# Performance work log

Measured on AMD Instinct MI355X. Metric: run time of the kernel, lower is better.

The kernel has to match this reference:

```python
import jax, jax.numpy as jnp
import numpy as np

B, N, C = 2, 2048, 768
H = 12
D = C // H
WINDOW = 129  # odd; half-window = 64
SCALE = D ** -0.5


def setup_inputs() -> dict:
    key = jax.random.key(0)
    k_x, k_qkv, k_proj, k_pb = jax.random.split(key, 4)
    x = jax.random.normal(k_x, (B, N, C), dtype=jnp.float32)
    # nn.Linear weights: stored as [out, in]; qkv_bias=False so no qkv bias
    w_qkv = jax.random.normal(k_qkv, (3 * C, C), dtype=jnp.float32) * (C ** -0.5)
    w_proj = jax.random.normal(k_proj, (C, C), dtype=jnp.float32) * (C ** -0.5)
    b_proj = jax.random.normal(k_pb, (C,), dtype=jnp.float32) * 0.01
    return {"x": x, "w_qkv": w_qkv, "w_proj": w_proj, "b_proj": b_proj}


def reference(x, w_qkv, w_proj, b_proj):
    b, n, c = x.shape
    # qkv projection: [B,N,3C] -> [3,B,H,N,D]
    qkv = jnp.einsum('bnc,ec->bne', x, w_qkv)
    qkv = qkv.reshape(b, n, 3, H, D).transpose(2, 0, 3, 1, 4)
    q, k, v = qkv[0], qkv[1], qkv[2]
    # dense scores then sliding-window mask (faithful to source)
    attn = jnp.einsum('bhnd,bhmd->bhnm', q, k) * SCALE
    half = WINDOW // 2
    idx = jnp.arange(n)
    mask = jnp.abs(idx[:, None] - idx[None, :]) <= half  # [N,N]
    attn = jnp.where(mask[None, None], attn, -jnp.inf)
    attn = jax.nn.softmax(attn, axis=-1)
    attn = jnp.nan_to_num(attn)
    out = jnp.einsum('bhnm,bhmd->bhnd', attn, v)  # [B,H,N,D]
    out = out.transpose(0, 2, 1, 3).reshape(b, n, c)
    out = jnp.einsum('bnc,oc->bno', out, w_proj) + b_proj
    return out
```

## Files before the change

kernel.cpp:

```cpp
#include <hip/hip_runtime.h>
#include <hip/hip_bf16.h>

#define Bsz   2
#define Nseq  2048
#define Cdim  768
#define E3    2304
#define Hh    12
#define Dd    64
#define HALF  64
#define SCALEF 0.125f

typedef __attribute__((ext_vector_type(8))) short short8;
typedef __attribute__((ext_vector_type(4))) float f32x4;

__device__ __forceinline__ unsigned short f2bf(float f) {
    unsigned int u = __float_as_uint(f);
    u = (u + 0x7FFFu + ((u >> 16) & 1u)) >> 16;
    return (unsigned short)u;
}
__device__ __forceinline__ unsigned int pk2(float a, float b) {
    __hip_bfloat162 h = __float22bfloat162_rn(make_float2(a, b));
    union { __hip_bfloat162 h2; unsigned int u; } cv; cv.h2 = h; return cv.u;
}
__device__ __forceinline__ uint4 cvt8(const float4& lo, const float4& hi) {
    return make_uint4(pk2(lo.x, lo.y), pk2(lo.z, lo.w),
                      pk2(hi.x, hi.y), pk2(hi.z, hi.w));
}

__device__ __forceinline__ void gl_lds16(const unsigned short* g, unsigned short* l) {
    __builtin_amdgcn_global_load_lds(
        (__attribute__((address_space(1))) void*)(g),
        (__attribute__((address_space(3))) void*)(l), 16, 0, 0);
}

__global__ __launch_bounds__(256) void cvt3(
    const float* __restrict__ x, const float* __restrict__ wq,
    const float* __restrict__ wp, unsigned short* __restrict__ xb,
    unsigned short* __restrict__ wqb, unsigned short* __restrict__ wpb)
{
    const int gid = blockIdx.x * 256 + threadIdx.x;
    const float* src; unsigned short* dst; int off;
    if (gid < 393216)      { src = x;  dst = xb;  off = gid; }
    else if (gid < 614400) { src = wq; dst = wqb; off = gid - 393216; }
    else                   { src = wp; dst = wpb; off = gid - 614400; }
    const float4 lo = *(const float4*)&src[(size_t)off * 8];
    const float4 hi = *(const float4*)&src[(size_t)off * 8 + 4];
    *(uint4*)&dst[(size_t)off * 8] = cvt8(lo, hi);
}

__global__ __launch_bounds__(256) void qkv_mfma(
    const unsigned short* __restrict__ xb, const unsigned short* __restrict__ wqb,
    unsigned short* __restrict__ qkvb)
{
    __shared__ __align__(16) unsigned short smem[16384];
    unsigned short* Asm = smem;
    unsigned short* Bsm = smem + 8192;

    const int t  = threadIdx.x;
    const int id = blockIdx.y * 18 + blockIdx.x;
    const int p8 = id & 7, j8 = id >> 3;
    const int wg = p8 * 72 + j8;
    const int by = wg / 18, bx = wg % 18;
    const int row0 = by * 128, col0 = bx * 128;

    const int lane = t & 63, wave = t >> 6;
    const int wm = wave >> 1, wn = wave & 1;
    const int ln = lane & 15, quad = lane >> 4;
    const int lr  = lane >> 3;
    const int sc  = ((lane ^ lr) & 7) * 8;
    const int xsw = (ln & 7) << 3;

    f32x4 acc[4][4] = {};

    for (int k0 = 0; k0 < Cdim; k0 += 64) {
        __syncthreads();
#pragma unroll
        for (int j = 0; j < 4; ++j) {
            gl_lds16(&xb[(size_t)(row0 + wave*32 + j*8 + lr) * Cdim + k0 + sc],
                     &Asm[(wave*4 + j) * 512]);
            gl_lds16(&wqb[(size_t)(col0 + wave*32 + j*8 + lr) * Cdim + k0 + sc],
                     &Bsm[(wave*4 + j) * 512]);
        }
        __syncthreads();
#pragma unroll
        for (int kk = 0; kk < 2; ++kk) {
            short8 af[4], bf[4];
#pragma unroll
            for (int mi = 0; mi < 4; ++mi)
                af[mi] = *(const short8*)&Asm[(wm*64 + mi*16 + ln)*64
                                              + ((kk*32 + quad*8) ^ xsw)];
#pragma unroll
            for (int ni = 0; ni < 4; ++ni)
                bf[ni] = *(const short8*)&Bsm[(wn*64 + ni*16 + ln)*64
                                              + ((kk*32 + quad*8) ^ xsw)];
#pragma unroll
            for (int mi = 0; mi < 4; ++mi)
#pragma unroll
                for (int ni = 0; ni < 4; ++ni)
                    acc[mi][ni] = __builtin_amdgcn_mfma_f32_16x16x32_bf16(
                        af[mi], bf[ni], acc[mi][ni], 0, 0, 0);
        }
    }

    unsigned short (*Cs)[72] = (unsigned short(*)[72])smem;
    const int rA = t >> 3, c8 = t & 7;
#pragma unroll
    for (int p = 0; p < 2; ++p) {
        __syncthreads();
        if (wn == p) {
#pragma unroll
            for (int mi = 0; mi < 4; ++mi)
#pragma unroll
                for (int ni = 0; ni < 4; ++ni)
#pragma unroll
                    for (int reg = 0; reg < 4; ++reg)
                        Cs[wm*64 + mi*16 + quad*4 + reg][ni*16 + ln] =
                            f2bf(acc[mi][ni][reg]);
        }
        __syncthreads();
#pragma unroll
        for (int j = 0; j < 4; ++j)
            *(uint4*)&qkvb[(size_t)(row0 + rA + j*32) * E3 + col0 + p*64 + c8*8] =
                *(const uint4*)&Cs[rA + j*32][c8*8];
    }
}

__global__ __launch_bounds__(256) void proj_mfma(
    const unsigned short* __restrict__ Ab, const unsigned short* __restrict__ wpb,
    const float* __restrict__ bias, float* __restrict__ out)
{
    __shared__ __align__(16) unsigned short smem[8192];
    unsigned short* Asm = smem;
    unsigned short* Bsm = smem + 4096;

    const int t  = threadIdx.x;
    const int id = blockIdx.y * 12 + blockIdx.x;
    const int p8 = id & 7, j2 = id >> 3;
    const int bx = j2 % 12;
    const int by = p8 * 8 + j2 / 12;
    const int row0 = by * 64, col0 = bx * 64;

    const int lane = t & 63, wave = t >> 6;
    const int ln = lane & 15, quad = lane >> 4;
    const int lr  = lane >> 3;
    const int sc  = ((lane ^ lr) & 7) * 8;
    const int xsw = (ln & 7) << 3;

    f32x4 acc[4] = {};

    for (int k0 = 0; k0 < Cdim; k0 += 64) {
        __syncthreads();
#pragma unroll
        for (int j = 0; j < 2; ++j) {
            const int r = wave*16 + j*8 + lr;
            gl_lds16(&Ab[(size_t)(row0 + r) * Cdim + k0 + sc],
                     &Asm[(wave*2 + j) * 512]);
            gl_lds16(&wpb[(size_t)(col0 + r) * Cdim + k0 + sc],
                     &Bsm[(wave*2 + j) * 512]);
        }
        __syncthreads();
#pragma unroll
        for (int kc = 0; kc < 2; ++kc) {
            short8 af = *(const short8*)&Asm[(wave*16 + ln)*64
                                             + ((kc*32 + quad*8) ^ xsw)];
#pragma unroll
            for (int ni = 0; ni < 4; ++ni) {
                short8 bf = *(const short8*)&Bsm[(ni*16 + ln)*64
                                                 + ((kc*32 + quad*8) ^ xsw)];
                acc[ni] = __builtin_amdgcn_mfma_f32_16x16x32_bf16(af, bf, acc[ni], 0, 0, 0);
            }
        }
    }

    float (*Csf)[36] = (float(*)[36])smem;
#pragma unroll
    for (int p = 0; p < 2; ++p) {
        __syncthreads();
#pragma unroll
        for (int ni = 0; ni < 2; ++ni) {
            const int nn = p * 2 + ni;
#pragma unroll
            for (int reg = 0; reg < 4; ++reg)
                Csf[wave*16 + quad*4 + reg][ni*16 + ln] = acc[nn][reg];
        }
        __syncthreads();
#pragma unroll
        for (int j = 0; j < 2; ++j) {
            const int F = t + j * 256, r = F >> 3, c4 = F & 7;
            const int col = col0 + p * 32 + c4 * 4;
            float4 v  = *(const float4*)&Csf[r][c4 * 4];
            float4 bv = *(const float4*)&bias[col];
            *(float4*)&out[(size_t)(row0 + r) * Cdim + col] =
                make_float4(v.x + bv.x, v.y + bv.y, v.z + bv.z, v.w + bv.w);
        }
    }
}

#define TQ2  64
#define KR   192
#define VSTn 200
#define PSTn 200

__global__ __launch_bounds__(256) void swin_attn(
    const unsigned short* __restrict__ qkvb, unsigned short* __restrict__ ab)
{
    __shared__ __align__(16) unsigned short SH[64 * VSTn];
    __shared__ __align__(16) unsigned short Pl[TQ2][PSTn];
    __shared__ float psum[TQ2];

    const int t  = threadIdx.x;
    const int id = blockIdx.y * 32 + blockIdx.x;
    const int p8 = id & 7, j8 = id >> 3;
    const int bh = j8 >> 2;
    const int i0 = (p8 * 4 + (j8 & 3)) * TQ2;
    const int b  = bh / Hh, h = bh % Hh;
    const int hoff = h * Dd;

    const int lane = t & 63, wave = t >> 6;
    const int ln = lane & 15, quad = lane >> 4;
    const int lr  = lane >> 3;
    const int scw = ((lane ^ lr) & 7) * 8;
    const int xsw = (ln & 7) << 3;
    const int rV  = t >> 3, c8 = t & 7;

    short8 qf[2];
#pragma unroll
    for (int kc = 0; kc < 2; ++kc)
        qf[kc] = *(const short8*)&qkvb[(size_t)(b * Nseq + i0 + wave*16 + ln) * E3
                                       + hoff + kc*32 + quad*8];

    uint4 vreg[6];
#pragma unroll
    for (int j = 0; j < 6; ++j) {
        int g = i0 - HALF + rV + j*32;
        g = min(max(g, 0), Nseq - 1);
        vreg[j] = *(const uint4*)&qkvb[(size_t)(b * Nseq + g) * E3 + 2*Cdim + hoff + c8*8];
    }

#pragma unroll
    for (int j = 0; j < 6; ++j) {
        const int base = (j*4 + wave) * 8;
        int g = i0 - HALF + base + lr;
        g = min(max(g, 0), Nseq - 1);
        gl_lds16(&qkvb[(size_t)(b * Nseq + g) * E3 + Cdim + hoff + scw],
                 &SH[base * 64]);
    }
    __syncthreads();

    f32x4 sacc[9] = {};
#pragma unroll
    for (int kc = 0; kc < 2; ++kc)
#pragma unroll
        for (int tt = 0; tt < 9; ++tt) {
            short8 kf = *(const short8*)&SH[((wave + tt)*16 + ln)*64
                                            + ((kc*32 + quad*8) ^ xsw)];
            sacc[tt] = __builtin_amdgcn_mfma_f32_16x16x32_bf16(qf[kc], kf, sacc[tt], 0, 0, 0);
        }

    float pm[4] = {-1e30f, -1e30f, -1e30f, -1e30f};
#pragma unroll
    for (int tt = 0; tt < 9; ++tt) {
        const int r = (wave + tt)*16 + ln;
        const int g = i0 - HALF + r;
#pragma unroll
        for (int reg = 0; reg < 4; ++reg) {
            const int q = wave*16 + quad*4 + reg;
            const bool valid = (r >= q) && (r <= q + 2*HALF) && (g >= 0) && (g < Nseq);
            const float s = valid ? sacc[tt][reg] * SCALEF : -1e30f;
            sacc[tt][reg] = s;
            pm[reg] = fmaxf(pm[reg], s);
        }
    }
#pragma unroll
    for (int reg = 0; reg < 4; ++reg) {
        pm[reg] = fmaxf(pm[reg], __shfl_xor(pm[reg], 1));
        pm[reg] = fmaxf(pm[reg], __shfl_xor(pm[reg], 2));
        pm[reg] = fmaxf(pm[reg], __shfl_xor(pm[reg], 4));
        pm[reg] = fmaxf(pm[reg], __shfl_xor(pm[reg], 8));
    }
    float ps[4] = {};
#pragma unroll
    for (int reg = 0; reg < 4; ++reg)
#pragma unroll
        for (int tt = 0; tt < 9; ++tt) {
            const float pv = (sacc[tt][reg] > -1e29f) ? __expf(sacc[tt][reg] - pm[reg]) : 0.f;
            sacc[tt][reg] = pv;
            ps[reg] += pv;
        }
#pragma unroll
    for (int reg = 0; reg < 4; ++reg) {
        ps[reg] += __shfl_xor(ps[reg], 1);
        ps[reg] += __shfl_xor(ps[reg], 2);
        ps[reg] += __shfl_xor(ps[reg], 4);
        ps[reg] += __shfl_xor(ps[reg], 8);
    }

#pragma unroll
    for (int tt = 0; tt < 9; ++tt)
#pragma unroll
        for (int reg = 0; reg < 4; ++reg)
            Pl[wave*16 + quad*4 + reg][(wave + tt)*16 + ln] = f2bf(sacc[tt][reg]);
    {
        const int tz = (wave & 1) ? (wave - 1) : (wave + 9);
        *(uint2*)&Pl[wave*16 + ln][tz*16 + quad*4] = make_uint2(0u, 0u);
    }
    if (ln == 0)
#pragma unroll
        for (int reg = 0; reg < 4; ++reg)
            psum[wave*16 + quad*4 + reg] = ps[reg];
    __syncthreads();

#pragma unroll
    for (int j = 0; j < 6; ++j) {
        const int r = rV + j*32;
        const int gr = ((r >> 3) ^ c8)*8 + (r & 7);
        union { unsigned short us[8]; uint4 u; } pk; pk.u = vreg[j];
#pragma unroll
        for (int d8 = 0; d8 < 8; ++d8)
            SH[(c8*8 + d8)*VSTn + gr] = pk.us[d8];
    }
    __syncthreads();

    const int kc0 = wave >> 1;
    f32x4 oacc[4] = {};
#pragma unroll
    for (int c = 0; c < 5; ++c) {
        const int kc = kc0 + c;
        short8 pf = *(const short8*)&Pl[wave*16 + ln][kc*32 + quad*8];
#pragma unroll
        for (int m = 0; m < 4; ++m) {
            const int d = m*16 + ln;
            short8 vf = *(const short8*)&SH[d * VSTn
                                            + (((kc*4 + quad) ^ (d >> 3)) << 3)];
            oacc[m] = __builtin_amdgcn_mfma_f32_16x16x32_bf16(vf, pf, oacc[m], 0, 0, 0);
        }
    }

    const int q = wave*16 + ln;
    const float inv = 1.f / psum[q];
    unsigned short* orow = &ab[(size_t)(b * Nseq + i0 + q) * Cdim + hoff];
#pragma unroll
    for (int m = 0; m < 4; ++m) {
        const int d0 = m*16 + quad*4;
        union { unsigned short us[4]; uint2 u2; } pk;
#pragma unroll
        for (int reg = 0; reg < 4; ++reg)
            pk.us[reg] = f2bf(oacc[m][reg] * inv);
        *(uint2*)&orow[d0] = pk.u2;
    }
}

extern "C" void kernel_launch(void* const* d_in, const int* in_sizes, int n_in,
                              void* d_out, int out_size, void* d_ws, size_t ws_size,
                              hipStream_t stream)
{
    const float* x      = (const float*)d_in[0];
    const float* w_qkv  = (const float*)d_in[1];
    const float* w_proj = (const float*)d_in[2];
    const float* b_proj = (const float*)d_in[3];
    float* out = (float*)d_out;

    unsigned short* qkvb = (unsigned short*)d_ws;
    unsigned short* ab   = qkvb + 9437184;
    unsigned short* xb   = ab   + 3145728;
    unsigned short* wqb  = xb   + 3145728;
    unsigned short* wpb  = wqb  + 1769472;

    cvt3<<<dim3(2688), 256, 0, stream>>>(x, w_qkv, w_proj, xb, wqb, wpb);
    qkv_mfma<<<dim3(18, 32), 256, 0, stream>>>(xb, wqb, qkvb);
    swin_attn<<<dim3(32, Bsz * Hh), 256, 0, stream>>>(qkvb, ab);
    proj_mfma<<<dim3(12, 64), 256, 0, stream>>>(ab, wpb, b_proj, out);
}
```

Measured before the change: 130.7 us.

## Double-buffer per-wave LDS staging in QKV and projection GEMMs without block barriers

```diff
diff --git a/kernel.cpp b/kernel.cpp
--- a/kernel.cpp
+++ b/kernel.cpp
@@ -13,6 +13,11 @@
 typedef __attribute__((ext_vector_type(8))) short short8;
 typedef __attribute__((ext_vector_type(4))) float f32x4;
 
+#define FENCE_LGKM() do {                                                  \
+    asm volatile("s_waitcnt lgkmcnt(0)" ::: "memory");                     \
+    __builtin_amdgcn_sched_barrier(0);                                     \
+} while (0)
+
 __device__ __forceinline__ unsigned short f2bf(float f) {
     unsigned int u = __float_as_uint(f);
     u = (u + 0x7FFFu + ((u >> 16) & 1u)) >> 16;
@@ -52,9 +57,7 @@
     const unsigned short* __restrict__ xb, const unsigned short* __restrict__ wqb,
     unsigned short* __restrict__ qkvb)
 {
-    __shared__ __align__(16) unsigned short smem[16384];
-    unsigned short* Asm = smem;
-    unsigned short* Bsm = smem + 8192;
+    __shared__ __align__(16) unsigned short smem[32768];
 
     const int t  = threadIdx.x;
     const int id = blockIdx.y * 18 + blockIdx.x;
@@ -66,42 +69,53 @@
     const int lane = t & 63, wave = t >> 6;
     const int wm = wave >> 1, wn = wave & 1;
     const int ln = lane & 15, quad = lane >> 4;
-    const int lr  = lane >> 3;
-    const int sc  = ((lane ^ lr) & 7) * 8;
-    const int xsw = (ln & 7) << 3;
+
+    const unsigned short* aSrc = &xb [(size_t)(row0 + wm*64 + (lane>>2)) * Cdim
+                                      + (lane&3)*8];
+    const unsigned short* bSrc = &wqb[(size_t)(col0 + wn*64 + (lane>>2)) * Cdim
+                                      + (lane&3)*8];
+    unsigned short* wl = &smem[wave * 8192];
 
     f32x4 acc[4][4] = {};
 
-    for (int k0 = 0; k0 < Cdim; k0 += 64) {
-        __syncthreads();
+    auto STAGE = [&](int tt) {
+        unsigned short* d = wl + (tt & 1) * 4096;
+        const int ko = tt * 32;
 #pragma unroll
         for (int j = 0; j < 4; ++j) {
-            gl_lds16(&xb[(size_t)(row0 + wave*32 + j*8 + lr) * Cdim + k0 + sc],
-                     &Asm[(wave*4 + j) * 512]);
-            gl_lds16(&wqb[(size_t)(col0 + wave*32 + j*8 + lr) * Cdim + k0 + sc],
-                     &Bsm[(wave*4 + j) * 512]);
-        }
-        __syncthreads();
-#pragma unroll
-        for (int kk = 0; kk < 2; ++kk) {
-            short8 af[4], bf[4];
-#pragma unroll
-            for (int mi = 0; mi < 4; ++mi)
-                af[mi] = *(const short8*)&Asm[(wm*64 + mi*16 + ln)*64
-                                              + ((kk*32 + quad*8) ^ xsw)];
+            gl_lds16(aSrc + ko + (size_t)(16*j) * Cdim, d + j*512);
+            gl_lds16(bSrc + ko + (size_t)(16*j) * Cdim, d + 2048 + j*512);
+        }
+    };
+    auto COMP = [&](int s) {
+        const unsigned short* ba = wl + s * 4096;
+        short8 af[4], bf[4];
+#pragma unroll
+        for (int mi = 0; mi < 4; ++mi)
+            af[mi] = *(const short8*)&ba[(mi*16 + ln)*32 + quad*8];
+#pragma unroll
+        for (int ni = 0; ni < 4; ++ni)
+            bf[ni] = *(const short8*)&ba[2048 + (ni*16 + ln)*32 + quad*8];
+#pragma unroll
+        for (int mi = 0; mi < 4; ++mi)
 #pragma unroll
             for (int ni = 0; ni < 4; ++ni)
-                bf[ni] = *(const short8*)&Bsm[(wn*64 + ni*16 + ln)*64
-                                              + ((kk*32 + quad*8) ^ xsw)];
-#pragma unroll
-            for (int mi = 0; mi < 4; ++mi)
-#pragma unroll
-                for (int ni = 0; ni < 4; ++ni)
-                    acc[mi][ni] = __builtin_amdgcn_mfma_f32_16x16x32_bf16(
-                        af[mi], bf[ni], acc[mi][ni], 0, 0, 0);
-        }
-    }
-
+                acc[mi][ni] = __builtin_amdgcn_mfma_f32_16x16x32_bf16(
+                    af[mi], bf[ni], acc[mi][ni], 0, 0, 0);
+    };
+
+    STAGE(0); STAGE(1);
+#pragma unroll
+    for (int k = 0; k < 24; ++k) {
+        if (k < 23) { asm volatile("s_waitcnt vmcnt(8)" ::: "memory"); }
+        else        { asm volatile("s_waitcnt vmcnt(0)" ::: "memory"); }
+        __builtin_amdgcn_sched_barrier(0);
+        COMP(k & 1);
+        FENCE_LGKM();
+        if (k + 2 < 24) STAGE(k + 2);
+    }
+
+    __syncthreads();
     unsigned short (*Cs)[72] = (unsigned short(*)[72])smem;
     const int rA = t >> 3, c8 = t & 7;
 #pragma unroll
@@ -129,9 +143,7 @@
     const unsigned short* __restrict__ Ab, const unsigned short* __restrict__ wpb,
     const float* __restrict__ bias, float* __restrict__ out)
 {
-    __shared__ __align__(16) unsigned short smem[8192];
-    unsigned short* Asm = smem;
-    unsigned short* Bsm = smem + 4096;
+    __shared__ __align__(16) unsigned short smem[20480];
 
     const int t  = threadIdx.x;
     const int id = blockIdx.y * 12 + blockIdx.x;
@@ -142,62 +154,58 @@
 
     const int lane = t & 63, wave = t >> 6;
     const int ln = lane & 15, quad = lane >> 4;
-    const int lr  = lane >> 3;
-    const int sc  = ((lane ^ lr) & 7) * 8;
-    const int xsw = (ln & 7) << 3;
+
+    const unsigned short* aSrc = &Ab [(size_t)(row0 + wave*16 + (lane>>2)) * Cdim
+                                      + (lane&3)*8];
+    const unsigned short* bSrc = &wpb[(size_t)(col0 + (lane>>2)) * Cdim
+                                      + (lane&3)*8];
+    unsigned short* wl = &smem[wave * 5120];
+
+    float bv[4];
+#pragma unroll
+    for (int ni = 0; ni < 4; ++ni)
+        bv[ni] = bias[col0 + ni*16 + ln];
 
     f32x4 acc[4] = {};
 
-    for (int k0 = 0; k0 < Cdim; k0 += 64) {
-        __syncthreads();
-#pragma unroll
-        for (int j = 0; j < 2; ++j) {
-            const int r = wave*16 + j*8 + lr;
-            gl_lds16(&Ab[(size_t)(row0 + r) * Cdim + k0 + sc],
-                     &Asm[(wave*2 + j) * 512]);
-            gl_lds16(&wpb[(size_t)(col0 + r) * Cdim + k0 + sc],
-                     &Bsm[(wave*2 + j) * 512]);
-        }
-        __syncthreads();
-#pragma unroll
-        for (int kc = 0; kc < 2; ++kc) {
-            short8 af = *(const short8*)&Asm[(wave*16 + ln)*64
-                                             + ((kc*32 + quad*8) ^ xsw)];
-#pragma unroll
-            for (int ni = 0; ni < 4; ++ni) {
-                short8 bf = *(const short8*)&Bsm[(ni*16 + ln)*64
-                                                 + ((kc*32 + quad*8) ^ xsw)];
-                acc[ni] = __builtin_amdgcn_mfma_f32_16x16x32_bf16(af, bf, acc[ni], 0, 0, 0);
-            }
-        }
-    }
-
-    float (*Csf)[36] = (float(*)[36])smem;
-#pragma unroll
-    for (int p = 0; p < 2; ++p) {
-        __syncthreads();
-#pragma unroll
-        for (int ni = 0; ni < 2; ++ni) {
-            const int nn = p * 2 + ni;
-#pragma unroll
-            for (int reg = 0; reg < 4; ++reg)
-                Csf[wave*16 + quad*4 + reg][ni*16 + ln] = acc[nn][reg];
-        }
-        __syncthreads();
-#pragma unroll
-        for (int j = 0; j < 2; ++j) {
-            const int F = t + j * 256, r = F >> 3, c4 = F & 7;
-            const int col = col0 + p * 32 + c4 * 4;
-            float4 v  = *(const float4*)&Csf[r][c4 * 4];
-            float4 bv = *(const float4*)&bias[col];
-            *(float4*)&out[(size_t)(row0 + r) * Cdim + col] =
-                make_float4(v.x + bv.x, v.y + bv.y, v.z + bv.z, v.w + bv.w);
-        }
-    }
+    auto STAGE = [&](int tt) {
+        unsigned short* d = wl + (tt & 1) * 2560;
+        const int ko = tt * 32;
+        gl_lds16(aSrc + ko, d);
+#pragma unroll
+        for (int j = 0; j < 4; ++j)
+            gl_lds16(bSrc + ko + (size_t)(16*j) * Cdim, d + 512 + j*512);
+    };
+    auto COMP = [&](int s) {
+        const unsigned short* ba = wl + s * 2560;
+        short8 af = *(const short8*)&ba[ln*32 + quad*8];
+#pragma unroll
+        for (int ni = 0; ni < 4; ++ni) {
+            short8 bf = *(const short8*)&ba[512 + (ni*16 + ln)*32 + quad*8];
+            acc[ni] = __builtin_amdgcn_mfma_f32_16x16x32_bf16(af, bf, acc[ni], 0, 0, 0);
+        }
+    };
+
+    STAGE(0); STAGE(1);
+#pragma unroll
+    for (int k = 0; k < 24; ++k) {
+        if (k < 23) { asm volatile("s_waitcnt vmcnt(5)" ::: "memory"); }
+        else        { asm volatile("s_waitcnt vmcnt(0)" ::: "memory"); }
+        __builtin_amdgcn_sched_barrier(0);
+        COMP(k & 1);
+        FENCE_LGKM();
+        if (k + 2 < 24) STAGE(k + 2);
+    }
+
+#pragma unroll
+    for (int ni = 0; ni < 4; ++ni)
+#pragma unroll
+        for (int reg = 0; reg < 4; ++reg)
+            out[(size_t)(row0 + wave*16 + quad*4 + reg) * Cdim
+                + col0 + ni*16 + ln] = acc[ni][reg] + bv[ni];
 }
 
 #define TQ2  64
-#define KR   192
 #define VSTn 200
 #define PSTn 200
 
```

Measured after the change: 135.9 us. 4.0% more time.
